# Optimization experiments

Hardware: AMD Instinct MI355X
Metric: run time of the kernel (lower is better)

Reference implementation:

```python
import jax, jax.numpy as jnp
import numpy as np

EPS = 1e-5

def _bn(t, gamma, beta):
    # training-mode BatchNorm2d: stats over (B,H,W), biased variance
    mean = jnp.mean(t, axis=(0, 2, 3), keepdims=True)
    var = jnp.var(t, axis=(0, 2, 3), keepdims=True)
    tn = (t - mean) * jax.lax.rsqrt(var + EPS)
    return tn * gamma[None, :, None, None] + beta[None, :, None, None]

def setup_inputs() -> dict:
    key = jax.random.key(0)
    ks = jax.random.split(key, 8)
    B, C, H, W = 16, 256, 64, 64
    u, k, v = 4, 16, 256
    s = 1.0 / np.sqrt(C)
    x = jax.random.normal(ks[0], (B, C, H, W), dtype=jnp.float32)
    Wq = jax.random.normal(ks[1], (k, C), dtype=jnp.float32) * s
    bq = jax.random.normal(ks[2], (k,), dtype=jnp.float32) * 0.01
    Wk = jax.random.normal(ks[3], (u * k, C), dtype=jnp.float32) * s
    bk = jax.random.normal(ks[4], (u * k,), dtype=jnp.float32) * 0.01
    Wv = jax.random.normal(ks[5], (u * v, C), dtype=jnp.float32) * s
    bv = jax.random.normal(ks[6], (u * v,), dtype=jnp.float32) * 0.01
    gamma_q = jnp.ones((k,), dtype=jnp.float32)
    beta_q = jnp.zeros((k,), dtype=jnp.float32)
    gamma_v = jnp.ones((u * v,), dtype=jnp.float32)
    beta_v = jnp.zeros((u * v,), dtype=jnp.float32)
    return {"x": x, "Wq": Wq, "bq": bq, "Wk": Wk, "bk": bk, "Wv": Wv, "bv": bv,
            "gamma_q": gamma_q, "beta_q": beta_q, "gamma_v": gamma_v, "beta_v": beta_v}

def reference(x, Wq, bq, Wk, bk, Wv, bv, gamma_q, beta_q, gamma_v, beta_v):
    B, C, H, W = x.shape
    k = Wq.shape[0]
    u = 4
    v = Wv.shape[0] // u
    # 1x1 convs as channel contractions
    Q = jnp.einsum('oc,bchw->bohw', Wq, x) + bq[None, :, None, None]   # [B,k,H,W]
    K = jnp.einsum('oc,bchw->bohw', Wk, x) + bk[None, :, None, None]   # [B,u*k,H,W]
    V = jnp.einsum('oc,bchw->bohw', Wv, x) + bv[None, :, None, None]   # [B,u*v,H,W]
    Q = _bn(Q, gamma_q, beta_q)
    V = _bn(V, gamma_v, beta_v)
    m = H * W
    Q = Q.reshape(B, k, m)          # [B,k,m]
    K = K.reshape(B, u, k, m)       # [B,u,k,m]
    V = V.reshape(B, u, v, m)       # [B,u,v,m]
    K = jax.nn.softmax(K, axis=3)
    context = jnp.einsum('bukm,buvm->bkv', K, V)   # [B,k,v]
    y = jnp.einsum('bkn,bkv->bvn', Q, context)     # [B,v,m]
    return y.reshape(B, v, H, W)
```

## Files before the change

kernel.cpp:

```cpp
#include <hip/hip_runtime.h>
#include <hip/hip_bf16.h>

typedef short s16x8 __attribute__((ext_vector_type(8)));
typedef short s16x4 __attribute__((ext_vector_type(4)));
typedef float f32x4 __attribute__((ext_vector_type(4)));
typedef unsigned u32;
typedef u32 u32x2 __attribute__((ext_vector_type(2)));

#define DI __device__ __forceinline__

constexpr int BB = 16;
constexpr int CC = 256;
constexpr int MM = 4096;
constexpr int KD = 16;
constexpr int UK = 64;
constexpr float EPSV = 1e-5f;

DI unsigned short f2bf(float f) {
  union { float f; unsigned u; } v; v.f = f;
  unsigned r = v.u + 0x7FFFu + ((v.u >> 16) & 1u);
  return (unsigned short)(r >> 16);
}
DI float bfu(unsigned short u) { union { u32 u; float f; } w; w.u = (u32)u << 16; return w.f; }
DI float bflo(u32 v) { union { u32 u; float f; } w; w.u = v << 16; return w.f; }
DI float bfhi(u32 v) { union { u32 u; float f; } w; w.u = v & 0xFFFF0000u; return w.f; }

__global__ __launch_bounds__(256) void k_cvt(const float* __restrict__ x,
    unsigned short* __restrict__ xbf, float* __restrict__ xsump) {
  int bid = blockIdx.x;
  size_t base = (size_t)bid * MM;
  int t = threadIdx.x;
  float s = 0.f;
#pragma unroll
  for (int i = 0; i < 4; ++i) {
    size_t idx = base + (size_t)(i * 256 + t) * 4;
    float4 v = *(const float4*)(x + idx);
    s16x4 c;
    c[0] = (short)f2bf(v.x); c[1] = (short)f2bf(v.y);
    c[2] = (short)f2bf(v.z); c[3] = (short)f2bf(v.w);
    *(s16x4*)&xbf[idx] = c;
    s += v.x + v.y + v.z + v.w;
  }
#pragma unroll
  for (int o = 32; o; o >>= 1) s += __shfl_down(s, o);
  __shared__ float red[4];
  if ((t & 63) == 0) red[t >> 6] = s;
  __syncthreads();
  if (t == 0) xsump[bid] = red[0] + red[1] + red[2] + red[3];
}

__global__ __launch_bounds__(512) void k_gxx(const unsigned short* __restrict__ xbf,
                                             u32* __restrict__ part) {
  int b = blockIdx.x >> 4, mc = blockIdx.x & 15;
  int m0 = mc * 256;
  __shared__ short lds[2][256 * 72];
  int t = threadIdx.x, w = t >> 6, l = t & 63;
  int wr = w >> 2, wc = w & 3;
  int lrow = l & 15, lk8 = (l >> 4) * 8;
  int srow = t >> 3, sseg = (t & 7) * 8;

  const unsigned short* gsrc = xbf + ((size_t)(b * CC + srow)) * MM + m0 + sseg;

  s16x8 rg[4];
#pragma unroll
  for (int i = 0; i < 4; ++i)
    rg[i] = *(const s16x8*)(gsrc + (size_t)i * 64 * MM);
#pragma unroll
  for (int i = 0; i < 4; ++i)
    *(s16x8*)&lds[0][(srow + i * 64) * 72 + sseg] = rg[i];

  f32x4 acc[8][4];
#pragma unroll
  for (int i = 0; i < 8; ++i)
#pragma unroll
    for (int j = 0; j < 4; ++j) acc[i][j] = (f32x4)0.f;

#pragma unroll
  for (int ks = 0; ks < 4; ++ks) {
    __syncthreads();
    if (ks < 3) {
#pragma unroll
      for (int i = 0; i < 4; ++i)
        rg[i] = *(const s16x8*)(gsrc + (size_t)i * 64 * MM + (ks + 1) * 64);
    }
    int buf = ks & 1;
#pragma unroll
    for (int half = 0; half < 2; ++half) {
      s16x8 af[8], bf[4];
#pragma unroll
      for (int i = 0; i < 8; ++i)
        af[i] = *(const s16x8*)&lds[buf][(wr * 128 + i * 16 + lrow) * 72 + half * 32 + lk8];
#pragma unroll
      for (int j = 0; j < 4; ++j)
        bf[j] = *(const s16x8*)&lds[buf][(wc * 64 + j * 16 + lrow) * 72 + half * 32 + lk8];
#pragma unroll
      for (int i = 0; i < 8; ++i)
#pragma unroll
        for (int j = 0; j < 4; ++j)
          acc[i][j] = __builtin_amdgcn_mfma_f32_16x16x32_bf16(af[i], bf[j], acc[i][j], 0, 0, 0);
    }
    if (ks < 3) {
#pragma unroll
      for (int i = 0; i < 4; ++i)
        *(s16x8*)&lds[buf ^ 1][(srow + i * 64) * 72 + sseg] = rg[i];
    }
  }

  size_t pb = (size_t)blockIdx.x * 32768;
#pragma unroll
  for (int i = 0; i < 8; ++i)
#pragma unroll
    for (int j = 0; j < 4; ++j) {
      int tau = (w * 8 + i) * 4 + j;
      u32x2 pk;
      pk[0] = (u32)f2bf(acc[i][j][0]) | ((u32)f2bf(acc[i][j][1]) << 16);
      pk[1] = (u32)f2bf(acc[i][j][2]) | ((u32)f2bf(acc[i][j][3]) << 16);
      *(u32x2*)&part[pb + tau * 128 + l * 2] = pk;
    }
}

__global__ __launch_bounds__(256) void k_gred(const u32* __restrict__ part,
                                              float* __restrict__ G) {
  int q = blockIdx.x * 256 + threadIdx.x;
  float s0 = 0.f, s1 = 0.f;
#pragma unroll 8
  for (int p = 0; p < 256; ++p) {
    u32 v = part[(size_t)p * 32768 + q];
    s0 += bflo(v);
    s1 += bfhi(v);
  }
  int r2 = q & 1, l = (q >> 1) & 63, tau = q >> 7;
  int j = tau & 3, i = (tau >> 2) & 7, w = tau >> 5;
  int wr = w >> 2, wc = w & 3;
  int row = wr * 128 + i * 16 + (l >> 4) * 4 + r2 * 2;
  int col = wc * 64 + j * 16 + (l & 15);
  G[row * 256 + col] = s0;
  G[(row + 1) * 256 + col] = s1;
}

__global__ __launch_bounds__(256) void k_proj(const unsigned short* __restrict__ xbf,
    const float* __restrict__ Wq, const float* __restrict__ bq,
    const float* __restrict__ Wk, const float* __restrict__ bk,
    unsigned short* __restrict__ Kbf, unsigned short* __restrict__ Qbf,
    float* __restrict__ pstat) {
  int b = blockIdx.x >> 5, mc = blockIdx.x & 31;
  int gm0 = mc * 128;
  __shared__ u32 xt[2][128 * 17];
  __shared__ short wb[2][80 * 40];
  __shared__ float smax[4][64], ssum[4][64];
  int t = threadIdx.x;
  int w = t >> 6, l = t & 63;
  int lrow = l & 15, lk = l >> 4;
  int c2 = t >> 4;
  int mq = t & 15;
  int wrow0 = t >> 3;
  int wcol = (t & 7) * 4;

  s16x4 xv[2][2];
  float4 wv[3];

  {
    const unsigned short* p0 = xbf + ((size_t)(b * CC + 2 * c2)) * MM + gm0 + mq * 4;
#pragma unroll
    for (int mb = 0; mb < 2; ++mb) {
      xv[mb][0] = *(const s16x4*)(p0 + mb * 64);
      xv[mb][1] = *(const s16x4*)(p0 + mb * 64 + MM);
    }
#pragma unroll
    for (int rep = 0; rep < 3; ++rep) {
      int row = rep * 32 + wrow0;
      if (row < 80)
        wv[rep] = *(const float4*)((row < 64 ? Wk + (size_t)row * CC
                                             : Wq + (size_t)(row - 64) * CC) + wcol);
    }
#pragma unroll
    for (int mb = 0; mb < 2; ++mb) {
      int m = mb * 64 + mq * 4;
#pragma unroll
      for (int i = 0; i < 4; ++i)
        xt[0][(m + i) * 17 + c2] =
            (u32)(unsigned short)xv[mb][0][i] | ((u32)(unsigned short)xv[mb][1][i] << 16);
    }
#pragma unroll
    for (int rep = 0; rep < 3; ++rep) {
      int row = rep * 32 + wrow0;
      if (row < 80) {
        s16x4 wc4;
        wc4[0] = (short)f2bf(wv[rep].x); wc4[1] = (short)f2bf(wv[rep].y);
        wc4[2] = (short)f2bf(wv[rep].z); wc4[3] = (short)f2bf(wv[rep].w);
        *(s16x4*)&wb[0][row * 40 + wcol] = wc4;
      }
    }
  }
  __syncthreads();

  f32x4 acc[5][2];
#pragma unroll
  for (int i = 0; i < 5; ++i) { acc[i][0] = (f32x4)0.f; acc[i][1] = (f32x4)0.f; }

  for (int ks = 0; ks < 8; ++ks) {
    int buf = ks & 1;
    if (ks < 7) {
      int c0 = (ks + 1) * 32;
      const unsigned short* p0 = xbf + ((size_t)(b * CC + c0 + 2 * c2)) * MM + gm0 + mq * 4;
#pragma unroll
      for (int mb = 0; mb < 2; ++mb) {
        xv[mb][0] = *(const s16x4*)(p0 + mb * 64);
        xv[mb][1] = *(const s16x4*)(p0 + mb * 64 + MM);
      }
#pragma unroll
      for (int rep = 0; rep < 3; ++rep) {
        int row = rep * 32 + wrow0;
        if (row < 80)
          wv[rep] = *(const float4*)((row < 64 ? Wk + (size_t)row * CC
                                               : Wq + (size_t)(row - 64) * CC) + c0 + wcol);
      }
    }
    union { s16x8 v; u32 wd[4]; } bfr[2];
#pragma unroll
    for (int j = 0; j < 2; ++j) {
      int ml = w * 32 + j * 16 + lrow;
#pragma unroll
      for (int i = 0; i < 4; ++i) bfr[j].wd[i] = xt[buf][ml * 17 + lk * 4 + i];
    }
#pragma unroll
    for (int ot = 0; ot < 5; ++ot) {
      s16x8 af = *(const s16x8*)&wb[buf][(ot * 16 + lrow) * 40 + lk * 8];
      acc[ot][0] = __builtin_amdgcn_mfma_f32_16x16x32_bf16(af, bfr[0].v, acc[ot][0], 0, 0, 0);
      acc[ot][1] = __builtin_amdgcn_mfma_f32_16x16x32_bf16(af, bfr[1].v, acc[ot][1], 0, 0, 0);
    }
    if (ks < 7) {
#pragma unroll
      for (int mb = 0; mb < 2; ++mb) {
        int m = mb * 64 + mq * 4;
#pragma unroll
        for (int i = 0; i < 4; ++i)
          xt[buf ^ 1][(m + i) * 17 + c2] =
              (u32)(unsigned short)xv[mb][0][i] | ((u32)(unsigned short)xv[mb][1][i] << 16);
      }
#pragma unroll
      for (int rep = 0; rep < 3; ++rep) {
        int row = rep * 32 + wrow0;
        if (row < 80) {
          s16x4 wc4;
          wc4[0] = (short)f2bf(wv[rep].x); wc4[1] = (short)f2bf(wv[rep].y);
          wc4[2] = (short)f2bf(wv[rep].z); wc4[3] = (short)f2bf(wv[rep].w);
          *(s16x4*)&wb[buf ^ 1][row * 40 + wcol] = wc4;
        }
      }
    }
    __syncthreads();
  }

  int mcol = gm0 + w * 32 + lrow;
#pragma unroll
  for (int ot = 0; ot < 4; ++ot)
#pragma unroll
    for (int r = 0; r < 4; ++r) {
      int o = ot * 16 + lk * 4 + r;
      float bias = bk[o];
      unsigned short u0 = f2bf(acc[ot][0][r] + bias);
      unsigned short u1 = f2bf(acc[ot][1][r] + bias);
      size_t rowoff = ((size_t)(b * UK + o)) * MM;
      Kbf[rowoff + mcol] = u0;
      Kbf[rowoff + mcol + 16] = u1;
      float rv0 = bfu(u0), rv1 = bfu(u1);
      float mx = fmaxf(rv0, rv1);
      mx = fmaxf(mx, __shfl_xor(mx, 1));
      mx = fmaxf(mx, __shfl_xor(mx, 2));
      mx = fmaxf(mx, __shfl_xor(mx, 4));
      mx = fmaxf(mx, __shfl_xor(mx, 8));
      float se = __expf(rv0 - mx) + __expf(rv1 - mx);
      se += __shfl_xor(se, 1);
      se += __shfl_xor(se, 2);
      se += __shfl_xor(se, 4);
      se += __shfl_xor(se, 8);
      if (lrow == 0) { smax[w][o] = mx; ssum[w][o] = se; }
    }
#pragma unroll
  for (int r = 0; r < 4; ++r) {
    int oq = lk * 4 + r;
    float bias = bq[oq];
    size_t rowoff = ((size_t)(b * KD + oq)) * MM;
    Qbf[rowoff + mcol] = f2bf(acc[4][0][r] + bias);
    Qbf[rowoff + mcol + 16] = f2bf(acc[4][1][r] + bias);
  }
  __syncthreads();
  if (t < 64) {
    float m0_ = smax[0][t], m1_ = smax[1][t], m2_ = smax[2][t], m3_ = smax[3][t];
    float mm = fmaxf(fmaxf(m0_, m1_), fmaxf(m2_, m3_));
    float ss = ssum[0][t] * __expf(m0_ - mm) + ssum[1][t] * __expf(m1_ - mm) +
               ssum[2][t] * __expf(m2_ - mm) + ssum[3][t] * __expf(m3_ - mm);
    size_t po = ((size_t)blockIdx.x * 64 + t) * 2;
    pstat[po] = mm;
    pstat[po + 1] = ss;
  }
}

__global__ __launch_bounds__(64) void k_pmerge(const float* __restrict__ pstat,
    float* __restrict__ rmax, float* __restrict__ rsum) {
  int b = blockIdx.x, o = threadIdx.x;
  float mm = -3.4e38f;
#pragma unroll 8
  for (int mc = 0; mc < 32; ++mc)
    mm = fmaxf(mm, pstat[((size_t)((b * 32 + mc) * 64 + o)) * 2]);
  float ss = 0.f;
#pragma unroll 8
  for (int mc = 0; mc < 32; ++mc) {
    size_t po = ((size_t)((b * 32 + mc) * 64 + o)) * 2;
    ss += pstat[po + 1] * __expf(pstat[po] - mm);
  }
  rmax[b * 64 + o] = mm;
  rsum[b * 64 + o] = ss;
}

__global__ __launch_bounds__(256) void k_fin(const float* __restrict__ G,
    const float* __restrict__ xsump,
    const float* __restrict__ Wv, const float* __restrict__ bv,
    const float* __restrict__ gv, const float* __restrict__ btv,
    const float* __restrict__ Wq, const float* __restrict__ bq,
    const float* __restrict__ gq, const float* __restrict__ btq,
    float* __restrict__ AV, float* __restrict__ BVa,
    float* __restrict__ AQ, float* __restrict__ BQa) {
  int t = threadIdx.x, w = t >> 6, l = t & 63;
  int o0 = blockIdx.x * 4;
  __shared__ float lw[4][256];
#pragma unroll
  for (int oo = 0; oo < 4; ++oo) {
    int o = o0 + oo;
    lw[oo][t] = (o < 1024) ? Wv[(size_t)o * CC + t] : Wq[(size_t)(o - 1024) * CC + t];
  }
  __syncthreads();

  float4 w4[4];
#pragma unroll
  for (int oo = 0; oo < 4; ++oo) w4[oo] = *(const float4*)&lw[oo][4 * l];

  float qf[4] = {0.f, 0.f, 0.f, 0.f};
#pragma unroll 4
  for (int i = 0; i < 64; ++i) {
    int r = i * 4 + w;
    float4 g4 = *(const float4*)(G + (size_t)r * CC + 4 * l);
#pragma unroll
    for (int oo = 0; oo < 4; ++oo) {
      float d = g4.x * w4[oo].x + g4.y * w4[oo].y + g4.z * w4[oo].z + g4.w * w4[oo].w;
      qf[oo] = fmaf(lw[oo][r], d, qf[oo]);
    }
  }

  float xs = 0.f;
#pragma unroll
  for (int bb = 0; bb < 16; ++bb) xs += xsump[bb * 256 + t];
  float sx[4];
#pragma unroll
  for (int oo = 0; oo < 4; ++oo) sx[oo] = lw[oo][t] * xs;

#pragma unroll
  for (int oo = 0; oo < 4; ++oo)
#pragma unroll
    for (int od = 32; od; od >>= 1) {
      qf[oo] += __shfl_xor(qf[oo], od);
      sx[oo] += __shfl_xor(sx[oo], od);
    }
  __shared__ float rq[4][4], rs[4][4];
  if (l == 0)
#pragma unroll
    for (int oo = 0; oo < 4; ++oo) { rq[w][oo] = qf[oo]; rs[w][oo] = sx[oo]; }
  __syncthreads();
  if (t < 4) {
    int oo = t, o = o0 + oo;
    float q = rq[0][oo] + rq[1][oo] + rq[2][oo] + rq[3][oo];
    float s = rs[0][oo] + rs[1][oo] + rs[2][oo] + rs[3][oo];
    float bias, gamma, beta; float *pa, *pb;
    if (o < 1024) { bias = bv[o]; gamma = gv[o]; beta = btv[o]; pa = AV + o; pb = BVa + o; }
    else { int oi = o - 1024; bias = bq[oi]; gamma = gq[oi]; beta = btq[oi]; pa = AQ + oi; pb = BQa + oi; }
    const float invN = 1.f / 65536.f;
    float mean = s * invN + bias;
    float e2 = q * invN + 2.f * bias * s * invN + bias * bias;
    float var = e2 - mean * mean;
    float a = gamma * rsqrtf(var + EPSV);
    *pa = a;
    *pb = beta - mean * a;
  }
}

__global__ __launch_bounds__(256) void k_xp(const unsigned short* __restrict__ xbf,
    const unsigned short* __restrict__ Kbf, const float* __restrict__ rmax,
    float* __restrict__ xpp) {
  int b = blockIdx.x >> 4, kc = blockIdx.x & 15;
  int kbase = kc * 256;
  __shared__ short la[2][64 * 40];
  __shared__ short lb[2][256 * 40];
  int t = threadIdx.x, w = t >> 6, l = t & 63;
  int lrow = l & 15, lk = (l >> 4) * 8;
  int ra = t >> 2, sga = (t & 3) * 8;

  float rm = rmax[b * UK + ra];
  const unsigned short* ksrc = Kbf + ((size_t)(b * UK + ra)) * MM + kbase + sga;
  const unsigned short* xsrc = xbf + ((size_t)(b * CC + ra)) * MM + kbase + sga;

  s16x8 kv, xv[4];

  kv = *(const s16x8*)ksrc;
#pragma unroll
  for (int i = 0; i < 4; ++i)
    xv[i] = *(const s16x8*)(xsrc + (size_t)i * 64 * MM);
  {
    s16x8 ev;
#pragma unroll
    for (int i = 0; i < 8; ++i)
      ev[i] = (short)f2bf(__expf(bfu((unsigned short)kv[i]) - rm));
    *(s16x8*)&la[0][ra * 40 + sga] = ev;
#pragma unroll
    for (int i = 0; i < 4; ++i)
      *(s16x8*)&lb[0][(ra + i * 64) * 40 + sga] = xv[i];
  }
  __syncthreads();

  f32x4 acc[4][4];
#pragma unroll
  for (int i = 0; i < 4; ++i)
#pragma unroll
    for (int j = 0; j < 4; ++j) acc[i][j] = (f32x4)0.f;

  for (int ks = 0; ks < 8; ++ks) {
    int buf = ks & 1;
    if (ks < 7) {
      int k1 = (ks + 1) * 32;
      kv = *(const s16x8*)(ksrc + k1);
#pragma unroll
      for (int i = 0; i < 4; ++i)
        xv[i] = *(const s16x8*)(xsrc + (size_t)i * 64 * MM + k1);
    }
    s16x8 af[4], bfr[4];
#pragma unroll
    for (int i = 0; i < 4; ++i) af[i] = *(const s16x8*)&la[buf][(i * 16 + lrow) * 40 + lk];
#pragma unroll
    for (int j = 0; j < 4; ++j) bfr[j] = *(const s16x8*)&lb[buf][(w * 64 + j * 16 + lrow) * 40 + lk];
#pragma unroll
    for (int i = 0; i < 4; ++i)
#pragma unroll
      for (int j = 0; j < 4; ++j)
        acc[i][j] = __builtin_amdgcn_mfma_f32_16x16x32_bf16(af[i], bfr[j], acc[i][j], 0, 0, 0);
    if (ks < 7) {
      s16x8 ev;
#pragma unroll
      for (int i = 0; i < 8; ++i)
        ev[i] = (short)f2bf(__expf(bfu((unsigned short)kv[i]) - rm));
      *(s16x8*)&la[buf ^ 1][ra * 40 + sga] = ev;
#pragma unroll
      for (int i = 0; i < 4; ++i)
        *(s16x8*)&lb[buf ^ 1][(ra + i * 64) * 40 + sga] = xv[i];
    }
    __syncthreads();
  }

  float* dst = xpp + (size_t)blockIdx.x * UK * CC;
#pragma unroll
  for (int i = 0; i < 4; ++i)
#pragma unroll
    for (int j = 0; j < 4; ++j)
#pragma unroll
      for (int r = 0; r < 4; ++r) {
        int row = i * 16 + (l >> 4) * 4 + r;
        int col = w * 64 + j * 16 + lrow;
        dst[row * 256 + col] = acc[i][j][r];
      }
}

__global__ __launch_bounds__(256) void k_prep(const float* __restrict__ xpp,
    const float* __restrict__ rsum, const float* __restrict__ Wv,
    const float* __restrict__ AV, unsigned short* __restrict__ xpn,
    unsigned short* __restrict__ wvs) {
  int t = threadIdx.x;
  if (blockIdx.x < 256) {
    int b = blockIdx.x >> 4, kk = blockIdx.x & 15;
    unsigned short* dst = xpn + ((size_t)(b * 16 + kk)) * 1024;
#pragma unroll
    for (int u = 0; u < 4; ++u) {
      int row = u * 16 + kk;
      float s = 0.f;
#pragma unroll
      for (int kc = 0; kc < 16; ++kc)
        s += xpp[((size_t)(b * 16 + kc) * UK + row) * CC + t];
      s /= rsum[b * UK + row];
      dst[u * 256 + t] = f2bf(s);
    }
  } else {
    int ch = blockIdx.x - 256;
    float a = AV[ch];
    wvs[(size_t)ch * CC + t] = f2bf(a * Wv[(size_t)ch * CC + t]);
  }
}

__global__ __launch_bounds__(64) void k_ctx2(const unsigned short* __restrict__ xpn,
    const unsigned short* __restrict__ wvs,
    const float* __restrict__ AV, const float* __restrict__ bv,
    const float* __restrict__ BVa, float* __restrict__ CTX) {
  int mt = blockIdx.x >> 3, nt = blockIdx.x & 7;
  int m0 = mt * 32, n0 = nt * 32;
  int l = threadIdx.x;
  int lrow = l & 15, lk8 = (l >> 4) * 8;

  f32x4 acc[2][2];
#pragma unroll
  for (int i = 0; i < 2; ++i)
#pragma unroll
    for (int j = 0; j < 2; ++j) acc[i][j] = (f32x4)0.f;

#pragma unroll 4
  for (int k0 = 0; k0 < 1024; k0 += 32) {
    int u = k0 >> 8, c0 = k0 & 255;
    s16x8 a0 = *(const s16x8*)&xpn[(size_t)(m0 + lrow) * 1024 + k0 + lk8];
    s16x8 a1 = *(const s16x8*)&xpn[(size_t)(m0 + 16 + lrow) * 1024 + k0 + lk8];
    s16x8 b0 = *(const s16x8*)&wvs[(size_t)(u * 256 + n0 + lrow) * CC + c0 + lk8];
    s16x8 b1 = *(const s16x8*)&wvs[(size_t)(u * 256 + n0 + 16 + lrow) * CC + c0 + lk8];
    acc[0][0] = __builtin_amdgcn_mfma_f32_16x16x32_bf16(a0, b0, acc[0][0], 0, 0, 0);
    acc[0][1] = __builtin_amdgcn_mfma_f32_16x16x32_bf16(a0, b1, acc[0][1], 0, 0, 0);
    acc[1][0] = __builtin_amdgcn_mfma_f32_16x16x32_bf16(a1, b0, acc[1][0], 0, 0, 0);
    acc[1][1] = __builtin_amdgcn_mfma_f32_16x16x32_bf16(a1, b1, acc[1][1], 0, 0, 0);
  }

  float cst[2];
#pragma unroll
  for (int j = 0; j < 2; ++j) {
    int vv = n0 + j * 16 + lrow;
    float s = 0.f;
#pragma unroll
    for (int u = 0; u < 4; ++u) {
      int ch = u * 256 + vv;
      s += AV[ch] * bv[ch] + BVa[ch];
    }
    cst[j] = s;
  }

#pragma unroll
  for (int i = 0; i < 2; ++i)
#pragma unroll
    for (int j = 0; j < 2; ++j)
#pragma unroll
      for (int r = 0; r < 4; ++r) {
        int row = m0 + i * 16 + (l >> 4) * 4 + r;
        int col = n0 + j * 16 + lrow;
        CTX[(size_t)row * 256 + col] = acc[i][j][r] + cst[j];
      }
}

__global__ __launch_bounds__(256) void k_y(const unsigned short* __restrict__ Qbf,
    const float* __restrict__ CTX,
    const float* __restrict__ AQ, const float* __restrict__ BQa,
    float* __restrict__ y) {
  int b = blockIdx.x >> 4, nc = blockIdx.x & 15;
  int m = nc * 256 + threadIdx.x;
  float qn[16];
#pragma unroll
  for (int kk = 0; kk < 16; ++kk)
    qn[kk] = AQ[kk] * bfu(Qbf[((size_t)b * KD + kk) * MM + m]) + BQa[kk];
  const float* cb = CTX + (size_t)b * KD * 256;
  float* yo = y + (size_t)b * 256 * MM + m;
#pragma unroll 4
  for (int vv = 0; vv < 256; ++vv) {
    float acc = 0.f;
#pragma unroll
    for (int kk = 0; kk < 16; ++kk)
      acc = fmaf(qn[kk], cb[kk * 256 + vv], acc);
    yo[(size_t)vv * MM] = acc;
  }
}

extern "C" void kernel_launch(void* const* d_in, const int* in_sizes, int n_in,
                              void* d_out, int out_size, void* d_ws, size_t ws_size,
                              hipStream_t stream) {
  const float* x   = (const float*)d_in[0];
  const float* Wq  = (const float*)d_in[1];
  const float* bq  = (const float*)d_in[2];
  const float* Wk  = (const float*)d_in[3];
  const float* bk  = (const float*)d_in[4];
  const float* Wv  = (const float*)d_in[5];
  const float* bv  = (const float*)d_in[6];
  const float* gq  = (const float*)d_in[7];
  const float* btq = (const float*)d_in[8];
  const float* gv  = (const float*)d_in[9];
  const float* btv = (const float*)d_in[10];
  float* out = (float*)d_out;
  float* ws  = (float*)d_ws;

  float* G     = ws;
  float* XSUMP = ws + 65536;
  float* PSTAT = ws + 69632;
  float* RMAX  = ws + 135168;
  float* RSUM  = ws + 136192;
  float* AV    = ws + 137216;
  float* BVa   = ws + 138240;
  float* AQ    = ws + 139264;
  float* BQa   = ws + 139280;
  float* CTX   = ws + 139520;
  u32*  PART   = (u32*)(ws + 205056);
  float* XPP   = ws + 205056;
  unsigned short* KBf = (unsigned short*)(ws + 4399360);
  unsigned short* QBf = (unsigned short*)(ws + 6496512);
  unsigned short* XBF = (unsigned short*)(ws + 8593664);
  unsigned short* XPN = (unsigned short*)(ws + 16982272);
  unsigned short* WVS = (unsigned short*)(ws + 17113344);

  k_cvt   <<<4096, 256, 0, stream>>>(x, XBF, XSUMP);
  k_gxx   <<<256,  512, 0, stream>>>(XBF, PART);
  k_gred  <<<128,  256, 0, stream>>>(PART, G);
  k_proj  <<<512,  256, 0, stream>>>(XBF, Wq, bq, Wk, bk, KBf, QBf, PSTAT);
  k_pmerge<<<16,   64,  0, stream>>>(PSTAT, RMAX, RSUM);
  k_fin   <<<260,  256, 0, stream>>>(G, XSUMP, Wv, bv, gv, btv, Wq, bq, gq, btq,
                                     AV, BVa, AQ, BQa);
  k_xp    <<<256,  256, 0, stream>>>(XBF, KBf, RMAX, XPP);
  k_prep  <<<1280, 256, 0, stream>>>(XPP, RSUM, Wv, AV, XPN, WVS);
  k_ctx2  <<<64,   64,  0, stream>>>(XPN, WVS, AV, bv, BVa, CTX);
  k_y     <<<256,  256, 0, stream>>>(QBf, CTX, AQ, BQa, out);
}
```

Baseline: 143.5 us.

## Fold softmax stat merge into consumers and store bf16 packed partials

```diff
diff --git a/kernel.cpp b/kernel.cpp
--- a/kernel.cpp
+++ b/kernel.cpp
@@ -297,23 +297,6 @@
   }
 }
 
-__global__ __launch_bounds__(64) void k_pmerge(const float* __restrict__ pstat,
-    float* __restrict__ rmax, float* __restrict__ rsum) {
-  int b = blockIdx.x, o = threadIdx.x;
-  float mm = -3.4e38f;
-#pragma unroll 8
-  for (int mc = 0; mc < 32; ++mc)
-    mm = fmaxf(mm, pstat[((size_t)((b * 32 + mc) * 64 + o)) * 2]);
-  float ss = 0.f;
-#pragma unroll 8
-  for (int mc = 0; mc < 32; ++mc) {
-    size_t po = ((size_t)((b * 32 + mc) * 64 + o)) * 2;
-    ss += pstat[po + 1] * __expf(pstat[po] - mm);
-  }
-  rmax[b * 64 + o] = mm;
-  rsum[b * 64 + o] = ss;
-}
-
 __global__ __launch_bounds__(256) void k_fin(const float* __restrict__ G,
     const float* __restrict__ xsump,
     const float* __restrict__ Wv, const float* __restrict__ bv,
@@ -385,17 +368,27 @@
 }
 
 __global__ __launch_bounds__(256) void k_xp(const unsigned short* __restrict__ xbf,
-    const unsigned short* __restrict__ Kbf, const float* __restrict__ rmax,
-    float* __restrict__ xpp) {
+    const unsigned short* __restrict__ Kbf, const float* __restrict__ pstat,
+    u32* __restrict__ xpph) {
   int b = blockIdx.x >> 4, kc = blockIdx.x & 15;
   int kbase = kc * 256;
   __shared__ short la[2][64 * 40];
   __shared__ short lb[2][256 * 40];
+  __shared__ float lrm[64];
   int t = threadIdx.x, w = t >> 6, l = t & 63;
   int lrow = l & 15, lk = (l >> 4) * 8;
   int ra = t >> 2, sga = (t & 3) * 8;
 
-  float rm = rmax[b * UK + ra];
+  if (t < 64) {
+    float mm = -3.4e38f;
+#pragma unroll 8
+    for (int mc2 = 0; mc2 < 32; ++mc2)
+      mm = fmaxf(mm, pstat[((size_t)((b * 32 + mc2) * 64 + t)) * 2]);
+    lrm[t] = mm;
+  }
+  __syncthreads();
+  float rm = lrm[ra];
+
   const unsigned short* ksrc = Kbf + ((size_t)(b * UK + ra)) * MM + kbase + sga;
   const unsigned short* xsrc = xbf + ((size_t)(b * CC + ra)) * MM + kbase + sga;
 
@@ -455,35 +448,57 @@
     __syncthreads();
   }
 
-  float* dst = xpp + (size_t)blockIdx.x * UK * CC;
+  u32* dst = xpph + (size_t)blockIdx.x * 8192;
 #pragma unroll
   for (int i = 0; i < 4; ++i)
 #pragma unroll
-    for (int j = 0; j < 4; ++j)
-#pragma unroll
-      for (int r = 0; r < 4; ++r) {
-        int row = i * 16 + (l >> 4) * 4 + r;
-        int col = w * 64 + j * 16 + lrow;
-        dst[row * 256 + col] = acc[i][j][r];
-      }
-}
-
-__global__ __launch_bounds__(256) void k_prep(const float* __restrict__ xpp,
-    const float* __restrict__ rsum, const float* __restrict__ Wv,
+    for (int j = 0; j < 4; ++j) {
+      int tau = (w * 4 + i) * 4 + j;
+      u32x2 pk;
+      pk[0] = (u32)f2bf(acc[i][j][0]) | ((u32)f2bf(acc[i][j][1]) << 16);
+      pk[1] = (u32)f2bf(acc[i][j][2]) | ((u32)f2bf(acc[i][j][3]) << 16);
+      *(u32x2*)&dst[tau * 128 + l * 2] = pk;
+    }
+}
+
+__global__ __launch_bounds__(256) void k_prep(const u32* __restrict__ xpph,
+    const float* __restrict__ pstat, const float* __restrict__ Wv,
     const float* __restrict__ AV, unsigned short* __restrict__ xpn,
     unsigned short* __restrict__ wvs) {
   int t = threadIdx.x;
   if (blockIdx.x < 256) {
     int b = blockIdx.x >> 4, kk = blockIdx.x & 15;
+    __shared__ float lrs[4];
+    if (t < 4) {
+      int row = t * 16 + kk;
+      float mm = -3.4e38f;
+#pragma unroll 8
+      for (int mc = 0; mc < 32; ++mc)
+        mm = fmaxf(mm, pstat[((size_t)((b * 32 + mc) * 64 + row)) * 2]);
+      float ss = 0.f;
+#pragma unroll 8
+      for (int mc = 0; mc < 32; ++mc) {
+        size_t po = ((size_t)((b * 32 + mc) * 64 + row)) * 2;
+        ss += pstat[po + 1] * __expf(pstat[po] - mm);
+      }
+      lrs[t] = ss;
+    }
+    __syncthreads();
     unsigned short* dst = xpn + ((size_t)(b * 16 + kk)) * 1024;
+    int w2 = t >> 6, j = (t >> 4) & 3, lrow = t & 15;
 #pragma unroll
     for (int u = 0; u < 4; ++u) {
       int row = u * 16 + kk;
+      int i = row >> 4, g = (row & 15) >> 2, r = row & 3;
+      int tau = (w2 * 4 + i) * 4 + j;
+      int idx = tau * 128 + (g * 16 + lrow) * 2 + (r >> 1);
       float s = 0.f;
 #pragma unroll
-      for (int kc = 0; kc < 16; ++kc)
-        s += xpp[((size_t)(b * 16 + kc) * UK + row) * CC + t];
-      s /= rsum[b * UK + row];
+      for (int kc = 0; kc < 16; ++kc) {
+        u32 v = xpph[(size_t)(b * 16 + kc) * 8192 + idx];
+        s += (r & 1) ? bfhi(v) : bflo(v);
+      }
+      s /= lrs[u];
       dst[u * 256 + t] = f2bf(s);
     }
   } else {
@@ -588,30 +603,27 @@
   float* G     = ws;
   float* XSUMP = ws + 65536;
   float* PSTAT = ws + 69632;
-  float* RMAX  = ws + 135168;
-  float* RSUM  = ws + 136192;
   float* AV    = ws + 137216;
   float* BVa   = ws + 138240;
   float* AQ    = ws + 139264;
   float* BQa   = ws + 139280;
   float* CTX   = ws + 139520;
   u32*  PART   = (u32*)(ws + 205056);
-  float* XPP   = ws + 205056;
+  u32*  XPPH   = (u32*)(ws + 205056);
   unsigned short* KBf = (unsigned short*)(ws + 4399360);
   unsigned short* QBf = (unsigned short*)(ws + 6496512);
   unsigned short* XBF = (unsigned short*)(ws + 8593664);
   unsigned short* XPN = (unsigned short*)(ws + 16982272);
   unsigned short* WVS = (unsigned short*)(ws + 17113344);
 
-  k_cvt   <<<4096, 256, 0, stream>>>(x, XBF, XSUMP);
-  k_gxx   <<<256,  512, 0, stream>>>(XBF, PART);
-  k_gred  <<<128,  256, 0, stream>>>(PART, G);
-  k_proj  <<<512,  256, 0, stream>>>(XBF, Wq, bq, Wk, bk, KBf, QBf, PSTAT);
-  k_pmerge<<<16,   64,  0, stream>>>(PSTAT, RMAX, RSUM);
-  k_fin   <<<260,  256, 0, stream>>>(G, XSUMP, Wv, bv, gv, btv, Wq, bq, gq, btq,
-                                     AV, BVa, AQ, BQa);
-  k_xp    <<<256,  256, 0, stream>>>(XBF, KBf, RMAX, XPP);
-  k_prep  <<<1280, 256, 0, stream>>>(XPP, RSUM, Wv, AV, XPN, WVS);
-  k_ctx2  <<<64,   64,  0, stream>>>(XPN, WVS, AV, bv, BVa, CTX);
-  k_y     <<<256,  256, 0, stream>>>(QBf, CTX, AQ, BQa, out);
-}
+  k_cvt  <<<4096, 256, 0, stream>>>(x, XBF, XSUMP);
+  k_gxx  <<<256,  512, 0, stream>>>(XBF, PART);
+  k_gred <<<128,  256, 0, stream>>>(PART, G);
+  k_proj <<<512,  256, 0, stream>>>(XBF, Wq, bq, Wk, bk, KBf, QBf, PSTAT);
+  k_fin  <<<260,  256, 0, stream>>>(G, XSUMP, Wv, bv, gv, btv, Wq, bq, gq, btq,
+                                    AV, BVa, AQ, BQa);
+  k_xp   <<<256,  256, 0, stream>>>(XBF, KBf, PSTAT, XPPH);
+  k_prep <<<1280, 256, 0, stream>>>(XPPH, PSTAT, Wv, AV, XPN, WVS);
+  k_ctx2 <<<64,   64,  0, stream>>>(XPN, WVS, AV, bv, BVa, CTX);
+  k_y    <<<256,  256, 0, stream>>>(QBf, CTX, AQ, BQa, out);
+}
```

Result: slower. 147.3 us (+2.6%).

## Emit transposed bf16 copy of x in convert kernel; projection reads it directly

Applied to the files above, without the earlier changes.

```diff
diff --git a/kernel.cpp b/kernel.cpp
--- a/kernel.cpp
+++ b/kernel.cpp
@@ -26,146 +26,63 @@
 DI float bfhi(u32 v) { union { u32 u; float f; } w; w.u = v & 0xFFFF0000u; return w.f; }
 
 __global__ __launch_bounds__(256) void k_cvt(const float* __restrict__ x,
-    unsigned short* __restrict__ xbf, float* __restrict__ xsump) {
-  int bid = blockIdx.x;
-  size_t base = (size_t)bid * MM;
-  int t = threadIdx.x;
-  float s = 0.f;
-#pragma unroll
-  for (int i = 0; i < 4; ++i) {
-    size_t idx = base + (size_t)(i * 256 + t) * 4;
-    float4 v = *(const float4*)(x + idx);
-    s16x4 c;
-    c[0] = (short)f2bf(v.x); c[1] = (short)f2bf(v.y);
-    c[2] = (short)f2bf(v.z); c[3] = (short)f2bf(v.w);
-    *(s16x4*)&xbf[idx] = c;
-    s += v.x + v.y + v.z + v.w;
-  }
-#pragma unroll
-  for (int o = 32; o; o >>= 1) s += __shfl_down(s, o);
-  __shared__ float red[4];
-  if ((t & 63) == 0) red[t >> 6] = s;
+    unsigned short* __restrict__ xbf, unsigned short* __restrict__ xbt,
+    float* __restrict__ xsump2) {
+  int b = blockIdx.x >> 6, cc = (blockIdx.x >> 4) & 3, mcb = blockIdx.x & 15;
+  int c0 = cc * 64, m0 = mcb * 256;
+  __shared__ short lt[64 * 266];
+  int t = threadIdx.x, w = t >> 6, l = t & 63;
+
+#pragma unroll
+  for (int r = 0; r < 16; ++r) {
+    int cr = w * 16 + r;
+    int c = c0 + cr;
+    size_t gidx = ((size_t)(b * CC + c)) * MM + m0 + l * 4;
+    float4 v = *(const float4*)(x + gidx);
+    s16x4 cv;
+    cv[0] = (short)f2bf(v.x); cv[1] = (short)f2bf(v.y);
+    cv[2] = (short)f2bf(v.z); cv[3] = (short)f2bf(v.w);
+    *(s16x4*)&xbf[gidx] = cv;
+    u32 lo = (u32)(unsigned short)cv[0] | ((u32)(unsigned short)cv[1] << 16);
+    u32 hi = (u32)(unsigned short)cv[2] | ((u32)(unsigned short)cv[3] << 16);
+    *(u32*)&lt[cr * 266 + l * 4]     = lo;
+    *(u32*)&lt[cr * 266 + l * 4 + 2] = hi;
+    float s = v.x + v.y + v.z + v.w;
+#pragma unroll
+    for (int o = 32; o; o >>= 1) s += __shfl_down(s, o);
+    if (l == 0) xsump2[c * 256 + b * 16 + mcb] = s;
+  }
   __syncthreads();
-  if (t == 0) xsump[bid] = red[0] + red[1] + red[2] + red[3];
-}
-
-__global__ __launch_bounds__(512) void k_gxx(const unsigned short* __restrict__ xbf,
-                                             u32* __restrict__ part) {
-  int b = blockIdx.x >> 4, mc = blockIdx.x & 15;
-  int m0 = mc * 256;
-  __shared__ short lds[2][256 * 72];
-  int t = threadIdx.x, w = t >> 6, l = t & 63;
-  int wr = w >> 2, wc = w & 3;
-  int lrow = l & 15, lk8 = (l >> 4) * 8;
-  int srow = t >> 3, sseg = (t & 7) * 8;
-
-  const unsigned short* gsrc = xbf + ((size_t)(b * CC + srow)) * MM + m0 + sseg;
-
-  s16x8 rg[4];
-#pragma unroll
-  for (int i = 0; i < 4; ++i)
-    rg[i] = *(const s16x8*)(gsrc + (size_t)i * 64 * MM);
-#pragma unroll
-  for (int i = 0; i < 4; ++i)
-    *(s16x8*)&lds[0][(srow + i * 64) * 72 + sseg] = rg[i];
-
-  f32x4 acc[8][4];
-#pragma unroll
-  for (int i = 0; i < 8; ++i)
-#pragma unroll
-    for (int j = 0; j < 4; ++j) acc[i][j] = (f32x4)0.f;
-
-#pragma unroll
-  for (int ks = 0; ks < 4; ++ks) {
-    __syncthreads();
-    if (ks < 3) {
-#pragma unroll
-      for (int i = 0; i < 4; ++i)
-        rg[i] = *(const s16x8*)(gsrc + (size_t)i * 64 * MM + (ks + 1) * 64);
-    }
-    int buf = ks & 1;
-#pragma unroll
-    for (int half = 0; half < 2; ++half) {
-      s16x8 af[8], bf[4];
-#pragma unroll
-      for (int i = 0; i < 8; ++i)
-        af[i] = *(const s16x8*)&lds[buf][(wr * 128 + i * 16 + lrow) * 72 + half * 32 + lk8];
-#pragma unroll
-      for (int j = 0; j < 4; ++j)
-        bf[j] = *(const s16x8*)&lds[buf][(wc * 64 + j * 16 + lrow) * 72 + half * 32 + lk8];
-#pragma unroll
-      for (int i = 0; i < 8; ++i)
-#pragma unroll
-        for (int j = 0; j < 4; ++j)
-          acc[i][j] = __builtin_amdgcn_mfma_f32_16x16x32_bf16(af[i], bf[j], acc[i][j], 0, 0, 0);
-    }
-    if (ks < 3) {
-#pragma unroll
-      for (int i = 0; i < 4; ++i)
-        *(s16x8*)&lds[buf ^ 1][(srow + i * 64) * 72 + sseg] = rg[i];
-    }
-  }
-
-  size_t pb = (size_t)blockIdx.x * 32768;
-#pragma unroll
-  for (int i = 0; i < 8; ++i)
-#pragma unroll
-    for (int j = 0; j < 4; ++j) {
-      int tau = (w * 8 + i) * 4 + j;
-      u32x2 pk;
-      pk[0] = (u32)f2bf(acc[i][j][0]) | ((u32)f2bf(acc[i][j][1]) << 16);
-      pk[1] = (u32)f2bf(acc[i][j][2]) | ((u32)f2bf(acc[i][j][3]) << 16);
-      *(u32x2*)&part[pb + tau * 128 + l * 2] = pk;
-    }
-}
-
-__global__ __launch_bounds__(256) void k_gred(const u32* __restrict__ part,
-                                              float* __restrict__ G) {
-  int q = blockIdx.x * 256 + threadIdx.x;
-  float s0 = 0.f, s1 = 0.f;
-#pragma unroll 8
-  for (int p = 0; p < 256; ++p) {
-    u32 v = part[(size_t)p * 32768 + q];
-    s0 += bflo(v);
-    s1 += bfhi(v);
-  }
-  int r2 = q & 1, l = (q >> 1) & 63, tau = q >> 7;
-  int j = tau & 3, i = (tau >> 2) & 7, w = tau >> 5;
-  int wr = w >> 2, wc = w & 3;
-  int row = wr * 128 + i * 16 + (l >> 4) * 4 + r2 * 2;
-  int col = wc * 64 + j * 16 + (l & 15);
-  G[row * 256 + col] = s0;
-  G[(row + 1) * 256 + col] = s1;
-}
-
-__global__ __launch_bounds__(256) void k_proj(const unsigned short* __restrict__ xbf,
+  int m = m0 + t;
+#pragma unroll
+  for (int k = 0; k < 8; ++k) {
+    s16x8 o8;
+#pragma unroll
+    for (int i = 0; i < 8; ++i) o8[i] = lt[(k * 8 + i) * 266 + t];
+    *(s16x8*)&xbt[((size_t)b * MM + m) * CC + c0 + k * 8] = o8;
+  }
+}
+
+__global__ __launch_bounds__(256) void k_proj(const unsigned short* __restrict__ xbt,
     const float* __restrict__ Wq, const float* __restrict__ bq,
     const float* __restrict__ Wk, const float* __restrict__ bk,
     unsigned short* __restrict__ Kbf, unsigned short* __restrict__ Qbf,
     float* __restrict__ pstat) {
   int b = blockIdx.x >> 5, mc = blockIdx.x & 31;
   int gm0 = mc * 128;
-  __shared__ u32 xt[2][128 * 17];
   __shared__ short wb[2][80 * 40];
   __shared__ float smax[4][64], ssum[4][64];
-  int t = threadIdx.x;
-  int w = t >> 6, l = t & 63;
+  int t = threadIdx.x, w = t >> 6, l = t & 63;
   int lrow = l & 15, lk = l >> 4;
-  int c2 = t >> 4;
-  int mq = t & 15;
-  int wrow0 = t >> 3;
-  int wcol = (t & 7) * 4;
-
-  s16x4 xv[2][2];
+  int wrow0 = t >> 3, wcol = (t & 7) * 4;
+
+  const unsigned short* bsrc0 = xbt + ((size_t)b * MM + gm0 + w * 32 + lrow) * CC;
+  const unsigned short* bsrc1 = bsrc0 + 16 * CC;
+
   float4 wv[3];
+  s16x8 bcur[2], bnext[2];
 
   {
-    const unsigned short* p0 = xbf + ((size_t)(b * CC + 2 * c2)) * MM + gm0 + mq * 4;
-#pragma unroll
-    for (int mb = 0; mb < 2; ++mb) {
-      xv[mb][0] = *(const s16x4*)(p0 + mb * 64);
-      xv[mb][1] = *(const s16x4*)(p0 + mb * 64 + MM);
-    }
 #pragma unroll
     for (int rep = 0; rep < 3; ++rep) {
       int row = rep * 32 + wrow0;
@@ -173,14 +90,8 @@
         wv[rep] = *(const float4*)((row < 64 ? Wk + (size_t)row * CC
                                              : Wq + (size_t)(row - 64) * CC) + wcol);
     }
-#pragma unroll
-    for (int mb = 0; mb < 2; ++mb) {
-      int m = mb * 64 + mq * 4;
-#pragma unroll
-      for (int i = 0; i < 4; ++i)
-        xt[0][(m + i) * 17 + c2] =
-            (u32)(unsigned short)xv[mb][0][i] | ((u32)(unsigned short)xv[mb][1][i] << 16);
-    }
+    bcur[0] = *(const s16x8*)(bsrc0 + lk * 8);
+    bcur[1] = *(const s16x8*)(bsrc1 + lk * 8);
 #pragma unroll
     for (int rep = 0; rep < 3; ++rep) {
       int row = rep * 32 + wrow0;
@@ -202,12 +113,6 @@
     int buf = ks & 1;
     if (ks < 7) {
       int c0 = (ks + 1) * 32;
-      const unsigned short* p0 = xbf + ((size_t)(b * CC + c0 + 2 * c2)) * MM + gm0 + mq * 4;
-#pragma unroll
-      for (int mb = 0; mb < 2; ++mb) {
-        xv[mb][0] = *(const s16x4*)(p0 + mb * 64);
-        xv[mb][1] = *(const s16x4*)(p0 + mb * 64 + MM);
-      }
 #pragma unroll
       for (int rep = 0; rep < 3; ++rep) {
         int row = rep * 32 + wrow0;
@@ -215,29 +120,16 @@
           wv[rep] = *(const float4*)((row < 64 ? Wk + (size_t)row * CC
                                                : Wq + (size_t)(row - 64) * CC) + c0 + wcol);
       }
-    }
-    union { s16x8 v; u32 wd[4]; } bfr[2];
-#pragma unroll
-    for (int j = 0; j < 2; ++j) {
-      int ml = w * 32 + j * 16 + lrow;
-#pragma unroll
-      for (int i = 0; i < 4; ++i) bfr[j].wd[i] = xt[buf][ml * 17 + lk * 4 + i];
+      bnext[0] = *(const s16x8*)(bsrc0 + c0 + lk * 8);
+      bnext[1] = *(const s16x8*)(bsrc1 + c0 + lk * 8);
     }
 #pragma unroll
     for (int ot = 0; ot < 5; ++ot) {
       s16x8 af = *(const s16x8*)&wb[buf][(ot * 16 + lrow) * 40 + lk * 8];
-      acc[ot][0] = __builtin_amdgcn_mfma_f32_16x16x32_bf16(af, bfr[0].v, acc[ot][0], 0, 0, 0);
-      acc[ot][1] = __builtin_amdgcn_mfma_f32_16x16x32_bf16(af, bfr[1].v, acc[ot][1], 0, 0, 0);
+      acc[ot][0] = __builtin_amdgcn_mfma_f32_16x16x32_bf16(af, bcur[0], acc[ot][0], 0, 0, 0);
+      acc[ot][1] = __builtin_amdgcn_mfma_f32_16x16x32_bf16(af, bcur[1], acc[ot][1], 0, 0, 0);
     }
     if (ks < 7) {
-#pragma unroll
-      for (int mb = 0; mb < 2; ++mb) {
-        int m = mb * 64 + mq * 4;
-#pragma unroll
-        for (int i = 0; i < 4; ++i)
-          xt[buf ^ 1][(m + i) * 17 + c2] =
-              (u32)(unsigned short)xv[mb][0][i] | ((u32)(unsigned short)xv[mb][1][i] << 16);
-      }
 #pragma unroll
       for (int rep = 0; rep < 3; ++rep) {
         int row = rep * 32 + wrow0;
@@ -248,6 +140,8 @@
           *(s16x4*)&wb[buf ^ 1][row * 40 + wcol] = wc4;
         }
       }
+      bcur[0] = bnext[0];
+      bcur[1] = bnext[1];
     }
     __syncthreads();
   }
@@ -297,6 +191,95 @@
   }
 }
 
+__global__ __launch_bounds__(512) void k_gxx(const unsigned short* __restrict__ xbf,
+                                             u32* __restrict__ part) {
+  int b = blockIdx.x >> 4, mc = blockIdx.x & 15;
+  int m0 = mc * 256;
+  __shared__ short lds[2][256 * 72];
+  int t = threadIdx.x, w = t >> 6, l = t & 63;
+  int wr = w >> 2, wc = w & 3;
+  int lrow = l & 15, lk8 = (l >> 4) * 8;
+  int srow = t >> 3, sseg = (t & 7) * 8;
+
+  const unsigned short* gsrc = xbf + ((size_t)(b * CC + srow)) * MM + m0 + sseg;
+
+  s16x8 rg[4];
+#pragma unroll
+  for (int i = 0; i < 4; ++i)
+    rg[i] = *(const s16x8*)(gsrc + (size_t)i * 64 * MM);
+#pragma unroll
+  for (int i = 0; i < 4; ++i)
+    *(s16x8*)&lds[0][(srow + i * 64) * 72 + sseg] = rg[i];
+
+  f32x4 acc[8][4];
+#pragma unroll
+  for (int i = 0; i < 8; ++i)
+#pragma unroll
+    for (int j = 0; j < 4; ++j) acc[i][j] = (f32x4)0.f;
+
+#pragma unroll
+  for (int ks = 0; ks < 4; ++ks) {
+    __syncthreads();
+    if (ks < 3) {
+#pragma unroll
+      for (int i = 0; i < 4; ++i)
+        rg[i] = *(const s16x8*)(gsrc + (size_t)i * 64 * MM + (ks + 1) * 64);
+    }
+    int buf = ks & 1;
+#pragma unroll
+    for (int half = 0; half < 2; ++half) {
+      s16x8 af[8], bf[4];
+#pragma unroll
+      for (int i = 0; i < 8; ++i)
+        af[i] = *(const s16x8*)&lds[buf][(wr * 128 + i * 16 + lrow) * 72 + half * 32 + lk8];
+#pragma unroll
+      for (int j = 0; j < 4; ++j)
+        bf[j] = *(const s16x8*)&lds[buf][(wc * 64 + j * 16 + lrow) * 72 + half * 32 + lk8];
+#pragma unroll
+      for (int i = 0; i < 8; ++i)
+#pragma unroll
+        for (int j = 0; j < 4; ++j)
+          acc[i][j] = __builtin_amdgcn_mfma_f32_16x16x32_bf16(af[i], bf[j], acc[i][j], 0, 0, 0);
+    }
+    if (ks < 3) {
+#pragma unroll
+      for (int i = 0; i < 4; ++i)
+        *(s16x8*)&lds[buf ^ 1][(srow + i * 64) * 72 + sseg] = rg[i];
+    }
+  }
+
+  size_t pb = (size_t)blockIdx.x * 32768;
+#pragma unroll
+  for (int i = 0; i < 8; ++i)
+#pragma unroll
+    for (int j = 0; j < 4; ++j) {
+      int tau = (w * 8 + i) * 4 + j;
+      u32x2 pk;
+      pk[0] = (u32)f2bf(acc[i][j][0]) | ((u32)f2bf(acc[i][j][1]) << 16);
+      pk[1] = (u32)f2bf(acc[i][j][2]) | ((u32)f2bf(acc[i][j][3]) << 16);
+      *(u32x2*)&part[pb + tau * 128 + l * 2] = pk;
+    }
+}
+
+__global__ __launch_bounds__(256) void k_gred(const u32* __restrict__ part,
+                                              float* __restrict__ G) {
+  int q = blockIdx.x * 256 + threadIdx.x;
+  float s0 = 0.f, s1 = 0.f;
+#pragma unroll 8
+  for (int p = 0; p < 256; ++p) {
+    u32 v = part[(size_t)p * 32768 + q];
+    s0 += bflo(v);
+    s1 += bfhi(v);
+  }
+  int r2 = q & 1, l = (q >> 1) & 63, tau = q >> 7;
+  int j = tau & 3, i = (tau >> 2) & 7, w = tau >> 5;
+  int wr = w >> 2, wc = w & 3;
+  int row = wr * 128 + i * 16 + (l >> 4) * 4 + r2 * 2;
+  int col = wc * 64 + j * 16 + (l & 15);
+  G[row * 256 + col] = s0;
+  G[(row + 1) * 256 + col] = s1;
+}
+
 __global__ __launch_bounds__(64) void k_pmerge(const float* __restrict__ pstat,
     float* __restrict__ rmax, float* __restrict__ rsum) {
   int b = blockIdx.x, o = threadIdx.x;
@@ -315,7 +298,7 @@
 }
 
 __global__ __launch_bounds__(256) void k_fin(const float* __restrict__ G,
-    const float* __restrict__ xsump,
+    const float* __restrict__ xsump2,
     const float* __restrict__ Wv, const float* __restrict__ bv,
     const float* __restrict__ gv, const float* __restrict__ btv,
     const float* __restrict__ Wq, const float* __restrict__ bq,
@@ -349,8 +332,11 @@
   }
 
   float xs = 0.f;
-#pragma unroll
-  for (int bb = 0; bb < 16; ++bb) xs += xsump[bb * 256 + t];
+#pragma unroll 8
+  for (int p = 0; p < 64; ++p) {
+    float4 v4 = *(const float4*)(xsump2 + (size_t)t * 256 + p * 4);
+    xs += v4.x + v4.y + v4.z + v4.w;
+  }
   float sx[4];
 #pragma unroll
   for (int oo = 0; oo < 4; ++oo) sx[oo] = lw[oo][t] * xs;
@@ -585,30 +571,31 @@
   float* out = (float*)d_out;
   float* ws  = (float*)d_ws;
 
-  float* G     = ws;
-  float* XSUMP = ws + 65536;
-  float* PSTAT = ws + 69632;
-  float* RMAX  = ws + 135168;
-  float* RSUM  = ws + 136192;
-  float* AV    = ws + 137216;
-  float* BVa   = ws + 138240;
-  float* AQ    = ws + 139264;
-  float* BQa   = ws + 139280;
-  float* CTX   = ws + 139520;
-  u32*  PART   = (u32*)(ws + 205056);
-  float* XPP   = ws + 205056;
-  unsigned short* KBf = (unsigned short*)(ws + 4399360);
-  unsigned short* QBf = (unsigned short*)(ws + 6496512);
-  unsigned short* XBF = (unsigned short*)(ws + 8593664);
-  unsigned short* XPN = (unsigned short*)(ws + 16982272);
-  unsigned short* WVS = (unsigned short*)(ws + 17113344);
-
-  k_cvt   <<<4096, 256, 0, stream>>>(x, XBF, XSUMP);
+  float* G      = ws;
+  float* XSUMP2 = ws + 65536;
+  float* PSTAT  = ws + 131072;
+  float* RMAX   = ws + 196608;
+  float* RSUM   = ws + 197632;
+  float* AV     = ws + 198656;
+  float* BVa    = ws + 199680;
+  float* AQ     = ws + 200704;
+  float* BQa    = ws + 200720;
+  float* CTX    = ws + 200960;
+  unsigned short* XBT = (unsigned short*)(ws + 266496);
+  u32*  PART    = (u32*)(ws + 266496);
+  float* XPP    = ws + 266496;
+  unsigned short* XBF = (unsigned short*)(ws + 8655104);
+  unsigned short* XPN = (unsigned short*)(ws + 17043712);
+  unsigned short* WVS = (unsigned short*)(ws + 17174784);
+  unsigned short* KBf = (unsigned short*)(ws + 17305856);
+  unsigned short* QBf = (unsigned short*)(ws + 19403008);
+
+  k_cvt   <<<1024, 256, 0, stream>>>(x, XBF, XBT, XSUMP2);
+  k_proj  <<<512,  256, 0, stream>>>(XBT, Wq, bq, Wk, bk, KBf, QBf, PSTAT);
+  k_pmerge<<<16,   64,  0, stream>>>(PSTAT, RMAX, RSUM);
   k_gxx   <<<256,  512, 0, stream>>>(XBF, PART);
   k_gred  <<<128,  256, 0, stream>>>(PART, G);
-  k_proj  <<<512,  256, 0, stream>>>(XBF, Wq, bq, Wk, bk, KBf, QBf, PSTAT);
-  k_pmerge<<<16,   64,  0, stream>>>(PSTAT, RMAX, RSUM);
-  k_fin   <<<260,  256, 0, stream>>>(G, XSUMP, Wv, bv, gv, btv, Wq, bq, gq, btq,
+  k_fin   <<<260,  256, 0, stream>>>(G, XSUMP2, Wv, bv, gv, btv, Wq, bq, gq, btq,
                                      AV, BVa, AQ, BQa);
   k_xp    <<<256,  256, 0, stream>>>(XBF, KBf, RMAX, XPP);
   k_prep  <<<1280, 256, 0, stream>>>(XPP, RSUM, Wv, AV, XPN, WVS);
```

After: 174.4 us. +21.5%, slower.
